# Optimization experiments

Measured on AMD Instinct MI355X. Metric: run time of the kernel, lower is better.

## Reference

```python
import jax, jax.numpy as jnp
import numpy as np

DIM = 1024
HEADS = 16
NUM_EXPERTS = 8
TOP_K = 2
INNER = 4 * DIM
EPS = 1e-5
NEG = -1e9


def setup_inputs() -> dict:
    key = jax.random.key(0)
    ks = jax.random.split(key, 12)
    s = 0.02
    return {
        "x": jax.random.normal(ks[0], (4, 1024, DIM), dtype=jnp.float32),
        "qkv_w": jax.random.normal(ks[1], (DIM, 3 * DIM), dtype=jnp.float32) * s,
        "out_w": jax.random.normal(ks[2], (DIM, DIM), dtype=jnp.float32) * s,
        "out_b": jnp.zeros((DIM,), dtype=jnp.float32),
        "thresh": jnp.float32(-2.0),
        "ln1_g": jnp.ones((DIM,), dtype=jnp.float32),
        "ln1_b": jnp.zeros((DIM,), dtype=jnp.float32),
        "ln2_g": jnp.ones((DIM,), dtype=jnp.float32),
        "ln2_b": jnp.zeros((DIM,), dtype=jnp.float32),
        "gate_w": jax.random.normal(ks[3], (DIM, NUM_EXPERTS), dtype=jnp.float32) * s,
        "w1": jax.random.normal(ks[4], (NUM_EXPERTS, DIM, INNER), dtype=jnp.float32) * s,
        "b1": jnp.zeros((NUM_EXPERTS, INNER), dtype=jnp.float32),
        "w2": jax.random.normal(ks[5], (NUM_EXPERTS, INNER, DIM), dtype=jnp.float32) * s,
        "b2": jnp.zeros((NUM_EXPERTS, DIM), dtype=jnp.float32),
    }


def _layernorm(x, g, b):
    mu = jnp.mean(x, axis=-1, keepdims=True)
    var = jnp.mean(jnp.square(x - mu), axis=-1, keepdims=True)
    return (x - mu) * jax.lax.rsqrt(var + EPS) * g + b


def reference(x, qkv_w, out_w, out_b, thresh, ln1_g, ln1_b, ln2_g, ln2_b,
              gate_w, w1, b1, w2, b2):
    B, N, D = x.shape
    H = HEADS
    Dh = D // H
    scale = Dh ** -0.5

    # --- Sparse attention (pre-norm, eval mode: dropout off) ---
    h = _layernorm(x, ln1_g, ln1_b)
    qkv = h @ qkv_w                                   # [B,N,3D]
    q, k, v = jnp.split(qkv, 3, axis=-1)
    def heads(t):
        return t.reshape(B, N, H, Dh).transpose(0, 2, 1, 3)  # [B,H,N,Dh]
    q, k, v = heads(q), heads(k), heads(v)
    dots = jnp.einsum("bhid,bhjd->bhij", q, k) * scale
    dots = jnp.where(dots < thresh, jnp.float32(NEG), dots)  # learnable sparsity
    attn = jax.nn.softmax(dots, axis=-1)
    o = jnp.einsum("bhij,bhjd->bhid", attn, v)
    o = o.transpose(0, 2, 1, 3).reshape(B, N, D)
    x = x + o @ out_w + out_b

    # --- MoE FFN (pre-norm) ---
    h2 = _layernorm(x, ln2_g, ln2_b).reshape(-1, D)   # [T,D]
    T = h2.shape[0]
    logits = h2 @ gate_w                              # [T,E]
    probs = jax.nn.softmax(logits, axis=-1)
    aux_loss = NUM_EXPERTS * jnp.sum(probs.mean(0) * probs.sum(0))

    top_w, top_i = jax.lax.top_k(logits, TOP_K)       # [T,k]
    top_w = jax.nn.softmax(top_w, axis=-1)
    # dense combine weights: [T,E], zero for unselected experts
    combine = jnp.zeros((T, NUM_EXPERTS), dtype=h2.dtype)
    combine = combine.at[jnp.arange(T)[:, None], top_i].set(top_w)

    out = jnp.zeros_like(h2)
    for e in range(NUM_EXPERTS):
        y = jax.nn.gelu(h2 @ w1[e] + b1[e], approximate=False) @ w2[e] + b2[e]
        out = out + combine[:, e:e + 1] * y

    x = x + out.reshape(B, N, D)
    return x, aux_loss
```

## Files before the change

### kernel.cpp

```cpp
#include <hip/hip_runtime.h>
#include <math.h>

#define DIM 1024
#define THREE_DIM 3072
#define INNER 4096
#define NTOK 4096
#define NPAIR 8192
#define NEXP 8
#define MAXMB 72

typedef __attribute__((ext_vector_type(8))) short bf16x8;
typedef __attribute__((ext_vector_type(4))) float f32x4;

__device__ __forceinline__ unsigned short f2bf(float f){
    unsigned int x = __float_as_uint(f);
    unsigned int r = x + 0x7fffu + ((x >> 16) & 1u);
    return (unsigned short)(r >> 16);
}

__device__ __forceinline__ unsigned short us4c(ushort4 v, int i){
    return i == 0 ? v.x : (i == 1 ? v.y : (i == 2 ? v.z : v.w));
}

__device__ __forceinline__ void glds16(const void* g, void* l){
    __builtin_amdgcn_global_load_lds(
        (const __attribute__((address_space(1))) void*)g,
        (__attribute__((address_space(3))) void*)l, 16, 0, 0);
}

template<int WRITE_BF>
__global__ __launch_bounds__(256)
void ln_kernel(const float* __restrict__ X, const float* __restrict__ g,
               const float* __restrict__ b, float* __restrict__ outF,
               unsigned short* __restrict__ outB)
{
    int row = blockIdx.x;
    int t = threadIdx.x;
    const float4 v = *((const float4*)(X + (size_t)row*DIM) + t);
    float s = v.x + v.y + v.z + v.w;
    #pragma unroll
    for (int m = 1; m < 64; m <<= 1) s += __shfl_xor(s, m, 64);
    __shared__ float red[8];
    int wid = t >> 6, lane = t & 63;
    if (lane == 0) red[wid] = s;
    __syncthreads();
    float mu = (red[0]+red[1]+red[2]+red[3]) * (1.0f/DIM);
    float dx = v.x-mu, dy = v.y-mu, dz = v.z-mu, dw = v.w-mu;
    float s2 = dx*dx + dy*dy + dz*dz + dw*dw;
    #pragma unroll
    for (int m = 1; m < 64; m <<= 1) s2 += __shfl_xor(s2, m, 64);
    if (lane == 0) red[4+wid] = s2;
    __syncthreads();
    float var = (red[4]+red[5]+red[6]+red[7]) * (1.0f/DIM);
    float inv = rsqrtf(var + 1e-5f);
    const float4 gg = *((const float4*)g + t);
    const float4 bb = *((const float4*)b + t);
    float y0 = dx*inv*gg.x + bb.x;
    float y1 = dy*inv*gg.y + bb.y;
    float y2 = dz*inv*gg.z + bb.z;
    float y3 = dw*inv*gg.w + bb.w;
    if (outF){
        float4 o; o.x=y0; o.y=y1; o.z=y2; o.w=y3;
        *((float4*)(outF + (size_t)row*DIM) + t) = o;
    }
    if (WRITE_BF){
        ushort4 u; u.x=f2bf(y0); u.y=f2bf(y1); u.z=f2bf(y2); u.w=f2bf(y3);
        *((ushort4*)(outB + (size_t)row*DIM) + t) = u;
    }
}

template<int MODE>
__global__ __launch_bounds__(256)
void gemm_bf(const unsigned short* __restrict__ A,
             const unsigned short* __restrict__ BT,
             int K, int N,
             const float* __restrict__ bias, const float* __restrict__ resid,
             unsigned short* __restrict__ outB, float* __restrict__ outF)
{
    __shared__ __align__(16) unsigned short As[128*64];
    __shared__ __align__(16) unsigned short Bs[128*64];
    int t = threadIdx.x, lane = t & 63, wid = t >> 6;
    int m0 = blockIdx.y * 128, n0 = blockIdx.x * 128;
    size_t aoff[4], boff[4];
    #pragma unroll
    for (int it = 0; it < 4; ++it){
        int chunk = it*256 + wid*64 + lane;
        int r = chunk >> 3, c16 = chunk & 7;
        int c16s = c16 ^ (r & 7);
        aoff[it] = (size_t)(m0 + r)*K + (size_t)(c16s*8);
        boff[it] = (size_t)(n0 + r)*K + (size_t)(c16s*8);
    }
    int wm = wid >> 1, wn = wid & 1;
    f32x4 acc[4][4];
    #pragma unroll
    for (int mi = 0; mi < 4; ++mi)
        #pragma unroll
        for (int ni = 0; ni < 4; ++ni)
            #pragma unroll
            for (int q = 0; q < 4; ++q) acc[mi][ni][q] = 0.f;

    for (int k0 = 0; k0 < K; k0 += 64){
        __syncthreads();
        #pragma unroll
        for (int it = 0; it < 4; ++it){
            glds16(A  + aoff[it] + k0, As + (size_t)(it*256 + wid*64)*8);
            glds16(BT + boff[it] + k0, Bs + (size_t)(it*256 + wid*64)*8);
        }
        __syncthreads();
        bf16x8 af[4][2], bg[4][2];
        #pragma unroll
        for (int mi = 0; mi < 4; ++mi){
            int row = wm*64 + mi*16 + (lane & 15);
            #pragma unroll
            for (int ks = 0; ks < 2; ++ks){
                int cg = (ks*4 + (lane >> 4)) ^ (row & 7);
                af[mi][ks] = *(const bf16x8*)&As[row*64 + cg*8];
            }
        }
        #pragma unroll
        for (int ni = 0; ni < 4; ++ni){
            int row = wn*64 + ni*16 + (lane & 15);
            #pragma unroll
            for (int ks = 0; ks < 2; ++ks){
                int cg = (ks*4 + (lane >> 4)) ^ (row & 7);
                bg[ni][ks] = *(const bf16x8*)&Bs[row*64 + cg*8];
            }
        }
        #pragma unroll
        for (int ks = 0; ks < 2; ++ks)
            #pragma unroll
            for (int mi = 0; mi < 4; ++mi)
                #pragma unroll
                for (int ni = 0; ni < 4; ++ni)
                    acc[mi][ni] = __builtin_amdgcn_mfma_f32_16x16x32_bf16(
                                      af[mi][ks], bg[ni][ks], acc[mi][ni], 0, 0, 0);
    }
    #pragma unroll
    for (int mi = 0; mi < 4; ++mi){
        #pragma unroll
        for (int ni = 0; ni < 4; ++ni){
            int ccol = n0 + wn*64 + ni*16 + (lane & 15);
            #pragma unroll
            for (int j = 0; j < 4; ++j){
                int row = m0 + wm*64 + mi*16 + (lane >> 4)*4 + j;
                float v = acc[mi][ni][j];
                if (MODE == 0){
                    outB[(size_t)row*N + ccol] = f2bf(v);
                } else {
                    outF[(size_t)row*N + ccol] =
                        v + bias[ccol] + resid[(size_t)row*N + ccol];
                }
            }
        }
    }
}

__global__ __launch_bounds__(256)
void attn4_kernel(const unsigned short* __restrict__ qkv,
                  unsigned short* __restrict__ O,
                  const float* __restrict__ threshp)
{
    __shared__ __align__(16) unsigned short Qs[64*64];
    __shared__ __align__(16) unsigned short Ks[64*64];
    __shared__ __align__(16) unsigned short Vp[8*520];
    __shared__ __align__(16) unsigned short Ps[4*1024];

    int t = threadIdx.x, lane = t & 63, w = t >> 6;
    int arow = lane & 15, agrp = lane >> 4;
    int qt = blockIdx.x, hh = blockIdx.y, bb = blockIdx.z;
    int qrow0 = bb*1024 + qt*64;
    float thresh = threshp[0];

    #pragma unroll
    for (int it = 0; it < 2; ++it){
        int chunk = it*256 + w*64 + lane;
        int r = chunk >> 3, c16 = chunk & 7;
        glds16(qkv + (size_t)(qrow0+r)*3072 + hh*64 + ((c16 ^ (r & 7))*8),
               Qs + (size_t)(it*256 + w*64)*8);
    }
    __syncthreads();
    bf16x8 qf[2];
    {
        int row = w*16 + arow;
        #pragma unroll
        for (int s = 0; s < 2; ++s){
            int c = (s*4 + agrp) ^ (row & 7);
            qf[s] = *(const bf16x8*)&Qs[row*64 + c*8];
        }
    }

    float m_[4], l_[4];
    f32x4 acc[4];
    #pragma unroll
    for (int j = 0; j < 4; ++j){ m_[j] = -INFINITY; l_[j] = 0.f; }
    #pragma unroll
    for (int d4 = 0; d4 < 4; ++d4)
        #pragma unroll
        for (int j = 0; j < 4; ++j) acc[d4][j] = 0.f;

    for (int kt = 0; kt < 16; ++kt){
        __syncthreads();
        int krow0 = bb*1024 + kt*64;
        #pragma unroll
        for (int it = 0; it < 2; ++it){
            int chunk = it*256 + w*64 + lane;
            int r = chunk >> 3, c16 = chunk & 7;
            glds16(qkv + (size_t)(krow0+r)*3072 + 1024 + hh*64 + ((c16 ^ (r & 7))*8),
                   Ks + (size_t)(it*256 + w*64)*8);
        }
        if (t < 128){
            int jc = t & 7, d0 = (t >> 3) * 4;
            ushort4 u[8];
            #pragma unroll
            for (int jj = 0; jj < 8; ++jj)
                u[jj] = *(const ushort4*)(qkv + (size_t)(krow0 + jc*8 + jj)*3072
                                          + 2048 + hh*64 + d0);
            #pragma unroll
            for (int i = 0; i < 4; ++i){
                ushort4 a, b;
                a.x = us4c(u[0], i); a.y = us4c(u[1], i);
                a.z = us4c(u[2], i); a.w = us4c(u[3], i);
                b.x = us4c(u[4], i); b.y = us4c(u[5], i);
                b.z = us4c(u[6], i); b.w = us4c(u[7], i);
                *(ushort4*)&Vp[jc*520 + (d0+i)*8]     = a;
                *(ushort4*)&Vp[jc*520 + (d0+i)*8 + 4] = b;
            }
        }
        __syncthreads();

        f32x4 sv[4];
        #pragma unroll
        for (int n = 0; n < 4; ++n)
            #pragma unroll
            for (int j = 0; j < 4; ++j) sv[n][j] = 0.f;
        #pragma unroll
        for (int n = 0; n < 4; ++n){
            int krow = n*16 + arow;
            #pragma unroll
            for (int s = 0; s < 2; ++s){
                int c = (s*4 + agrp) ^ (krow & 7);
                bf16x8 kf = *(const bf16x8*)&Ks[krow*64 + c*8];
                sv[n] = __builtin_amdgcn_mfma_f32_16x16x32_bf16(qf[s], kf, sv[n], 0, 0, 0);
            }
        }
        #pragma unroll
        for (int n = 0; n < 4; ++n)
            #pragma unroll
            for (int j = 0; j < 4; ++j){
                float s = sv[n][j] * 0.125f;
                sv[n][j] = (s < thresh) ? -1e9f : s;
            }
        float tmax[4], fac[4], rsum[4];
        #pragma unroll
        for (int j = 0; j < 4; ++j)
            tmax[j] = fmaxf(fmaxf(sv[0][j], sv[1][j]), fmaxf(sv[2][j], sv[3][j]));
        #pragma unroll
        for (int msk = 1; msk < 16; msk <<= 1)
            #pragma unroll
            for (int j = 0; j < 4; ++j)
                tmax[j] = fmaxf(tmax[j], __shfl_xor(tmax[j], msk, 64));
        #pragma unroll
        for (int j = 0; j < 4; ++j){
            float mn = fmaxf(m_[j], tmax[j]);
            fac[j] = __expf(m_[j] - mn);
            m_[j] = mn;
        }
        #pragma unroll
        for (int n = 0; n < 4; ++n)
            #pragma unroll
            for (int j = 0; j < 4; ++j)
                sv[n][j] = __expf(sv[n][j] - m_[j]);
        #pragma unroll
        for (int j = 0; j < 4; ++j)
            rsum[j] = sv[0][j] + sv[1][j] + sv[2][j] + sv[3][j];
        #pragma unroll
        for (int msk = 1; msk < 16; msk <<= 1)
            #pragma unroll
            for (int j = 0; j < 4; ++j)
                rsum[j] += __shfl_xor(rsum[j], msk, 64);
        #pragma unroll
        for (int j = 0; j < 4; ++j)
            l_[j] = l_[j]*fac[j] + rsum[j];
        #pragma unroll
        for (int n = 0; n < 4; ++n){
            int col = n*16 + arow;
            #pragma unroll
            for (int j = 0; j < 4; ++j){
                int r = agrp*4 + j;
                int idx = r*64 + (((col>>3) ^ (r&7)) << 3) + (col & 7);
                Ps[w*1024 + idx] = f2bf(sv[n][j]);
            }
        }
        #pragma unroll
        for (int d4 = 0; d4 < 4; ++d4)
            #pragma unroll
            for (int j = 0; j < 4; ++j) acc[d4][j] *= fac[j];
        #pragma unroll
        for (int s = 0; s < 2; ++s){
            int c = (s*4 + agrp) ^ (arow & 7);
            bf16x8 pa = *(const bf16x8*)&Ps[w*1024 + arow*64 + c*8];
            int jc = s*4 + agrp;
            #pragma unroll
            for (int d4 = 0; d4 < 4; ++d4){
                int dcol = d4*16 + arow;
                bf16x8 vb = *(const bf16x8*)&Vp[jc*520 + dcol*8];
                acc[d4] = __builtin_amdgcn_mfma_f32_16x16x32_bf16(pa, vb, acc[d4], 0, 0, 0);
            }
        }
    }
    #pragma unroll
    for (int j = 0; j < 4; ++j){
        float inv = 1.0f / l_[j];
        int row = qrow0 + w*16 + agrp*4 + j;
        #pragma unroll
        for (int d4 = 0; d4 < 4; ++d4)
            O[(size_t)row*1024 + hh*64 + d4*16 + arow] = f2bf(acc[d4][j] * inv);
    }
}

__global__ __launch_bounds__(64)
void gate_kernel(const float* __restrict__ h2, const float* __restrict__ gw,
                 float* __restrict__ probs, int* __restrict__ top_i,
                 float* __restrict__ top_w)
{
    int tk = blockIdx.x;
    int lane = threadIdx.x;
    const float* hr = h2 + (size_t)tk*DIM;
    float acc[8];
    #pragma unroll
    for (int e = 0; e < 8; ++e) acc[e] = 0.f;
    for (int d = lane; d < DIM; d += 64){
        float hv = hr[d];
        const float* grow = gw + d*8;
        #pragma unroll
        for (int e = 0; e < 8; ++e) acc[e] = fmaf(hv, grow[e], acc[e]);
    }
    #pragma unroll
    for (int m = 1; m < 64; m <<= 1)
        #pragma unroll
        for (int e = 0; e < 8; ++e) acc[e] += __shfl_xor(acc[e], m, 64);
    if (lane == 0){
        float mx = acc[0];
        #pragma unroll
        for (int e = 1; e < 8; ++e) mx = fmaxf(mx, acc[e]);
        float p[8], s = 0.f;
        #pragma unroll
        for (int e = 0; e < 8; ++e){ p[e] = __expf(acc[e]-mx); s += p[e]; }
        float invs = 1.f/s;
        #pragma unroll
        for (int e = 0; e < 8; ++e) probs[(size_t)tk*8+e] = p[e]*invs;
        int i0 = 0; float v0 = acc[0];
        #pragma unroll
        for (int e = 1; e < 8; ++e) if (acc[e] > v0){ v0 = acc[e]; i0 = e; }
        int i1 = -1; float v1 = -INFINITY;
        #pragma unroll
        for (int e = 0; e < 8; ++e) if (e != i0 && acc[e] > v1){ v1 = acc[e]; i1 = e; }
        float w0 = 1.f/(1.f + __expf(v1 - v0));
        top_i[tk*2]   = i0; top_i[tk*2+1] = i1;
        top_w[tk*2]   = w0; top_w[tk*2+1] = 1.f - w0;
    }
}

__global__ __launch_bounds__(256)
void aux_kernel(const float* __restrict__ probs, float* __restrict__ dout)
{
    int t = threadIdx.x;
    float acc[8];
    #pragma unroll
    for (int e = 0; e < 8; ++e) acc[e] = 0.f;
    for (int r = t; r < NTOK; r += 256){
        const float* pr = probs + (size_t)r*8;
        #pragma unroll
        for (int e = 0; e < 8; ++e) acc[e] += pr[e];
    }
    #pragma unroll
    for (int m = 1; m < 64; m <<= 1)
        #pragma unroll
        for (int e = 0; e < 8; ++e) acc[e] += __shfl_xor(acc[e], m, 64);
    __shared__ float red[4][8];
    int wid = t >> 6, lane = t & 63;
    if (lane == 0)
        for (int e = 0; e < 8; ++e) red[wid][e] = acc[e];
    __syncthreads();
    if (t == 0){
        float aux = 0.f;
        for (int e = 0; e < 8; ++e){
            float S = red[0][e]+red[1][e]+red[2][e]+red[3][e];
            aux += S*S;
        }
        dout[(size_t)NTOK*DIM] = aux * (8.0f/NTOK);
    }
}

__global__ __launch_bounds__(512)
void routing_kernel(const int* __restrict__ topi, int* __restrict__ perm,
                    int* __restrict__ mblk_e)
{
    __shared__ int cnt[8];
    __shared__ int obase[8];
    int t = threadIdx.x, w = t >> 6, lane = t & 63;
    int c = 0;
    for (int i0 = 0; i0 < NPAIR; i0 += 64){
        int e = topi[i0 + lane];
        c += (e == w) ? 1 : 0;
    }
    #pragma unroll
    for (int m = 1; m < 64; m <<= 1) c += __shfl_xor(c, m, 64);
    if (lane == 0) cnt[w] = c;
    __syncthreads();
    if (t == 0){
        int mb = 0;
        for (int e = 0; e < 8; ++e){
            obase[e] = mb*128;
            int nb = (cnt[e] + 127) >> 7;
            for (int k = 0; k < nb; ++k) mblk_e[mb++] = e;
        }
        for (; mb < MAXMB; ++mb) mblk_e[mb] = -1;
    }
    __syncthreads();
    for (int i = t; i < MAXMB*128; i += 512) perm[i] = -1;
    __syncthreads();
    int base = obase[w];
    for (int i0 = 0; i0 < NPAIR; i0 += 64){
        int p = i0 + lane;
        int e = topi[p];
        bool mt = (e == w);
        unsigned long long mk = __ballot(mt);
        int rank = __popcll(mk & ((1ull << lane) - 1ull));
        if (mt) perm[base + rank] = p;
        base += __popcll(mk);
    }
}

template<int MODE>
__global__ __launch_bounds__(256)
void gemm_moe2(const unsigned short* __restrict__ Abase,
               const unsigned short* __restrict__ BTbase,
               int K, int N, int lda,
               const int* __restrict__ perm, const int* __restrict__ mblk_e,
               const float* __restrict__ bias,
               unsigned short* __restrict__ actout,
               const float* __restrict__ topw, float* __restrict__ dout)
{
    int mb = blockIdx.y;
    int e = mblk_e[mb];
    if (e < 0) return;
    __shared__ __align__(16) unsigned short As[128*64];
    __shared__ __align__(16) unsigned short Bs[128*64];
    __shared__ int permL[128];
    int t = threadIdx.x;
    if (t < 128) permL[t] = perm[mb*128 + t];
    __syncthreads();
    int lane = t & 63, wid = t >> 6;
    int n0 = blockIdx.x * 128;
    const unsigned short* BT = BTbase + (size_t)e * (size_t)N * (size_t)K;
    int base_chunk = wid*64 + lane;
    size_t aoff[4], boff[4];
    #pragma unroll
    for (int it = 0; it < 4; ++it){
        int chunk = base_chunk + it*256;
        int r = chunk >> 3, c16 = chunk & 7;
        int c16s = c16 ^ (r & 7);
        size_t ar;
        if (MODE == 2){ int p = permL[r]; ar = (p >= 0) ? (size_t)(p >> 1) : 0; }
        else          { ar = (size_t)(mb*128 + r); }
        aoff[it] = ar*(size_t)lda + (size_t)(c16s*8);
        boff[it] = (size_t)(n0 + r)*(size_t)K + (size_t)(c16s*8);
    }
    int wm = wid >> 1, wn = wid & 1;
    f32x4 acc[4][4];
    #pragma unroll
    for (int mi = 0; mi < 4; ++mi)
        #pragma unroll
        for (int ni = 0; ni < 4; ++ni)
            #pragma unroll
            for (int q = 0; q < 4; ++q) acc[mi][ni][q] = 0.f;

    for (int k0 = 0; k0 < K; k0 += 64){
        __syncthreads();
        #pragma unroll
        for (int it = 0; it < 4; ++it){
            glds16(Abase + aoff[it] + k0, As + (size_t)(wid*64 + it*256)*8);
            glds16(BT    + boff[it] + k0, Bs + (size_t)(wid*64 + it*256)*8);
        }
        __syncthreads();
        bf16x8 af[4][2], bg[4][2];
        #pragma unroll
        for (int mi = 0; mi < 4; ++mi){
            int row = wm*64 + mi*16 + (lane & 15);
            #pragma unroll
            for (int ks = 0; ks < 2; ++ks){
                int cg = (ks*4 + (lane >> 4)) ^ (row & 7);
                af[mi][ks] = *(const bf16x8*)&As[row*64 + cg*8];
            }
        }
        #pragma unroll
        for (int ni = 0; ni < 4; ++ni){
            int row = wn*64 + ni*16 + (lane & 15);
            #pragma unroll
            for (int ks = 0; ks < 2; ++ks){
                int cg = (ks*4 + (lane >> 4)) ^ (row & 7);
                bg[ni][ks] = *(const bf16x8*)&Bs[row*64 + cg*8];
            }
        }
        #pragma unroll
        for (int ks = 0; ks < 2; ++ks)
            #pragma unroll
            for (int mi = 0; mi < 4; ++mi)
                #pragma unroll
                for (int ni = 0; ni < 4; ++ni)
                    acc[mi][ni] = __builtin_amdgcn_mfma_f32_16x16x32_bf16(
                                      af[mi][ks], bg[ni][ks], acc[mi][ni], 0, 0, 0);
    }
    #pragma unroll
    for (int mi = 0; mi < 4; ++mi){
        #pragma unroll
        for (int ni = 0; ni < 4; ++ni){
            int ccol = n0 + wn*64 + ni*16 + (lane & 15);
            float bv = bias[(size_t)e*N + ccol];
            #pragma unroll
            for (int j = 0; j < 4; ++j){
                int rloc = wm*64 + mi*16 + (lane >> 4)*4 + j;
                float v = acc[mi][ni][j];
                if (MODE == 2){
                    float gx = v + bv;
                    float z2 = gx * fmaf(gx*gx, 0.07135481283f, 1.595769122f);
                    float ex = __expf(-z2);
                    float gl = gx * __builtin_amdgcn_rcpf(1.0f + ex);
                    actout[(size_t)(mb*128 + rloc)*N + ccol] = f2bf(gl);
                } else {
                    int p = permL[rloc];
                    if (p >= 0){
                        float val = (v + bv) * topw[p];
                        atomicAdd(&dout[(size_t)(p >> 1)*N + ccol], val);
                    }
                }
            }
        }
    }
}

__global__ __launch_bounds__(256)
void transp_cast(const float* __restrict__ W, unsigned short* __restrict__ WT,
                 int K, int N)
{
    __shared__ float tile[32][33];
    size_t base = (size_t)blockIdx.z * (size_t)K * (size_t)N;
    const float* Wp = W + base;
    unsigned short* Tp = WT + base;
    int t = threadIdx.x;
    int r = t >> 3, c4 = (t & 7) << 2;
    int n0 = blockIdx.x << 5, k0 = blockIdx.y << 5;
    float4 v = *(const float4*)(Wp + (size_t)(k0+r)*N + n0 + c4);
    tile[r][c4+0] = v.x; tile[r][c4+1] = v.y;
    tile[r][c4+2] = v.z; tile[r][c4+3] = v.w;
    __syncthreads();
    ushort4 u;
    u.x = f2bf(tile[c4+0][r]);
    u.y = f2bf(tile[c4+1][r]);
    u.z = f2bf(tile[c4+2][r]);
    u.w = f2bf(tile[c4+3][r]);
    *(ushort4*)(Tp + (size_t)(n0+r)*K + k0 + c4) = u;
}

extern "C" void kernel_launch(void* const* d_in, const int* in_sizes, int n_in,
                              void* d_out, int out_size, void* d_ws, size_t ws_size,
                              hipStream_t stream)
{
    const float* x      = (const float*)d_in[0];
    const float* qkv_w  = (const float*)d_in[1];
    const float* out_w  = (const float*)d_in[2];
    const float* out_b  = (const float*)d_in[3];
    const float* thresh = (const float*)d_in[4];
    const float* ln1_g  = (const float*)d_in[5];
    const float* ln1_b  = (const float*)d_in[6];
    const float* ln2_g  = (const float*)d_in[7];
    const float* ln2_b  = (const float*)d_in[8];
    const float* gate_w = (const float*)d_in[9];
    const float* w1     = (const float*)d_in[10];
    const float* b1     = (const float*)d_in[11];
    const float* w2     = (const float*)d_in[12];
    const float* b2     = (const float*)d_in[13];
    float* out = (float*)d_out;
    char* ws = (char*)d_ws;

    const size_t MB = (size_t)1 << 20;
    unsigned short* h1bf  = (unsigned short*)(ws);
    unsigned short* qkvbf = (unsigned short*)(ws + 8*MB);
    unsigned short* obf   = (unsigned short*)(ws + 32*MB);
    float*          h2    = (float*)(ws + 40*MB);
    unsigned short* h2bf  = (unsigned short*)(ws + 56*MB);
    unsigned short* qwT   = (unsigned short*)(ws + 64*MB);
    unsigned short* owT   = (unsigned short*)(ws + 70*MB);
    unsigned short* w1T   = (unsigned short*)(ws + 72*MB);
    unsigned short* w2T   = (unsigned short*)(ws + 136*MB);
    unsigned short* act   = (unsigned short*)(ws + 200*MB);
    float* probs          = (float*)(ws + 276*MB);
    int*   top_i          = (int*)(ws + 276*MB + 131072);
    float* top_w          = (float*)(ws + 276*MB + 163840);
    int*   perm           = (int*)(ws + 276*MB + 196608);
    int*   mblk           = (int*)(ws + 276*MB + 237568);

    transp_cast<<<dim3(THREE_DIM/32, DIM/32, 1), 256, 0, stream>>>(qkv_w, qwT, DIM, THREE_DIM);
    transp_cast<<<dim3(DIM/32, DIM/32, 1), 256, 0, stream>>>(out_w, owT, DIM, DIM);

    ln_kernel<1><<<NTOK, 256, 0, stream>>>(x, ln1_g, ln1_b, nullptr, h1bf);
    gemm_bf<0><<<dim3(THREE_DIM/128, NTOK/128), 256, 0, stream>>>(
        h1bf, qwT, DIM, THREE_DIM, nullptr, nullptr, qkvbf, nullptr);
    attn4_kernel<<<dim3(16, 16, 4), 256, 0, stream>>>(qkvbf, obf, thresh);
    gemm_bf<1><<<dim3(DIM/128, NTOK/128), 256, 0, stream>>>(
        obf, owT, DIM, DIM, out_b, x, nullptr, out);
    ln_kernel<1><<<NTOK, 256, 0, stream>>>(out, ln2_g, ln2_b, h2, h2bf);
    gate_kernel<<<NTOK, 64, 0, stream>>>(h2, gate_w, probs, top_i, top_w);
    aux_kernel<<<1, 256, 0, stream>>>(probs, out);
    routing_kernel<<<1, 512, 0, stream>>>(top_i, perm, mblk);

    transp_cast<<<dim3(INNER/32, DIM/32, NEXP), 256, 0, stream>>>(w1, w1T, DIM, INNER);
    transp_cast<<<dim3(DIM/32, INNER/32, NEXP), 256, 0, stream>>>(w2, w2T, INNER, DIM);

    gemm_moe2<2><<<dim3(INNER/128, MAXMB), 256, 0, stream>>>(
        h2bf, w1T, DIM, INNER, DIM, perm, mblk, b1, act, nullptr, nullptr);
    gemm_moe2<3><<<dim3(DIM/128, MAXMB), 256, 0, stream>>>(
        act, w2T, INNER, DIM, INNER, perm, mblk, b2, nullptr, top_w, out);
}
```

Measured before the change: 513.3 us.

## Swizzle block IDs across XCDs and split-K the MoE down-projection

Flattens the launch grids of the GEMMs and the attention kernel to 1D and remaps block IDs so that consecutive logical tiles land on the same XCD, aiming for better L2 reuse of shared A/B tiles across the MI355X's chiplets. The second MoE GEMM is also split along K into two halves, doubling its grid to improve occupancy. The split is safe because that GEMM already accumulates with atomics, and bias is added only by the first split. The cost is extra atomic traffic on the output and some index arithmetic per block.

Measured after the change: 553.1 us. 7.7% more time.

```diff
diff --git a/kernel.cpp b/kernel.cpp
--- a/kernel.cpp
+++ b/kernel.cpp
@@ -26,6 +26,11 @@
     __builtin_amdgcn_global_load_lds(
         (const __attribute__((address_space(1))) void*)g,
         (__attribute__((address_space(3))) void*)l, 16, 0, 0);
+}
+
+__device__ __forceinline__ int xcd_swz(){
+    int cpx = gridDim.x >> 3;
+    return (blockIdx.x & 7) * cpx + (blockIdx.x >> 3);
 }
 
 template<int WRITE_BF>
@@ -73,14 +78,16 @@
 __global__ __launch_bounds__(256)
 void gemm_bf(const unsigned short* __restrict__ A,
              const unsigned short* __restrict__ BT,
-             int K, int N,
+             int K, int N, int gnx,
              const float* __restrict__ bias, const float* __restrict__ resid,
              unsigned short* __restrict__ outB, float* __restrict__ outF)
 {
     __shared__ __align__(16) unsigned short As[128*64];
     __shared__ __align__(16) unsigned short Bs[128*64];
+    int fid = xcd_swz();
+    int nx = fid % gnx, my = fid / gnx;
+    int m0 = my * 128, n0 = nx * 128;
     int t = threadIdx.x, lane = t & 63, wid = t >> 6;
-    int m0 = blockIdx.y * 128, n0 = blockIdx.x * 128;
     size_t aoff[4], boff[4];
     #pragma unroll
     for (int it = 0; it < 4; ++it){
@@ -165,9 +172,10 @@
     __shared__ __align__(16) unsigned short Vp[8*520];
     __shared__ __align__(16) unsigned short Ps[4*1024];
 
+    int fid = xcd_swz();
+    int qt = fid & 15, hh = (fid >> 4) & 15, bb = fid >> 8;
     int t = threadIdx.x, lane = t & 63, w = t >> 6;
     int arow = lane & 15, agrp = lane >> 4;
-    int qt = blockIdx.x, hh = blockIdx.y, bb = blockIdx.z;
     int qrow0 = bb*1024 + qt*64;
     float thresh = threshp[0];
 
@@ -442,9 +450,17 @@
                unsigned short* __restrict__ actout,
                const float* __restrict__ topw, float* __restrict__ dout)
 {
-    int mb = blockIdx.y;
+    const int GNX = (MODE == 2) ? (INNER/128) : (DIM/128);
+    const int KSP = (MODE == 2) ? 1 : 2;
+    int fid = xcd_swz();
+    int nx = fid % GNX;
+    int rest = fid / GNX;
+    int mb = rest % MAXMB;
+    int kk = rest / MAXMB;
     int e = mblk_e[mb];
     if (e < 0) return;
+    int kspan = K / KSP, kbeg = kk * kspan, kend = kbeg + kspan;
+
     __shared__ __align__(16) unsigned short As[128*64];
     __shared__ __align__(16) unsigned short Bs[128*64];
     __shared__ int permL[128];
@@ -452,7 +468,7 @@
     if (t < 128) permL[t] = perm[mb*128 + t];
     __syncthreads();
     int lane = t & 63, wid = t >> 6;
-    int n0 = blockIdx.x * 128;
+    int n0 = nx * 128;
     const unsigned short* BT = BTbase + (size_t)e * (size_t)N * (size_t)K;
     int base_chunk = wid*64 + lane;
     size_t aoff[4], boff[4];
@@ -476,7 +492,7 @@
             #pragma unroll
             for (int q = 0; q < 4; ++q) acc[mi][ni][q] = 0.f;
 
-    for (int k0 = 0; k0 < K; k0 += 64){
+    for (int k0 = kbeg; k0 < kend; k0 += 64){
         __syncthreads();
         #pragma unroll
         for (int it = 0; it < 4; ++it){
@@ -517,7 +533,7 @@
         #pragma unroll
         for (int ni = 0; ni < 4; ++ni){
             int ccol = n0 + wn*64 + ni*16 + (lane & 15);
-            float bv = bias[(size_t)e*N + ccol];
+            float bv = (kk == 0) ? bias[(size_t)e*N + ccol] : 0.f;
             #pragma unroll
             for (int j = 0; j < 4; ++j){
                 int rloc = wm*64 + mi*16 + (lane >> 4)*4 + j;
@@ -605,11 +621,11 @@
     transp_cast<<<dim3(DIM/32, DIM/32, 1), 256, 0, stream>>>(out_w, owT, DIM, DIM);
 
     ln_kernel<1><<<NTOK, 256, 0, stream>>>(x, ln1_g, ln1_b, nullptr, h1bf);
-    gemm_bf<0><<<dim3(THREE_DIM/128, NTOK/128), 256, 0, stream>>>(
-        h1bf, qwT, DIM, THREE_DIM, nullptr, nullptr, qkvbf, nullptr);
-    attn4_kernel<<<dim3(16, 16, 4), 256, 0, stream>>>(qkvbf, obf, thresh);
-    gemm_bf<1><<<dim3(DIM/128, NTOK/128), 256, 0, stream>>>(
-        obf, owT, DIM, DIM, out_b, x, nullptr, out);
+    gemm_bf<0><<<(THREE_DIM/128)*(NTOK/128), 256, 0, stream>>>(
+        h1bf, qwT, DIM, THREE_DIM, THREE_DIM/128, nullptr, nullptr, qkvbf, nullptr);
+    attn4_kernel<<<16*16*4, 256, 0, stream>>>(qkvbf, obf, thresh);
+    gemm_bf<1><<<(DIM/128)*(NTOK/128), 256, 0, stream>>>(
+        obf, owT, DIM, DIM, DIM/128, out_b, x, nullptr, out);
     ln_kernel<1><<<NTOK, 256, 0, stream>>>(out, ln2_g, ln2_b, h2, h2bf);
     gate_kernel<<<NTOK, 64, 0, stream>>>(h2, gate_w, probs, top_i, top_w);
     aux_kernel<<<1, 256, 0, stream>>>(probs, out);
@@ -618,8 +634,8 @@
     transp_cast<<<dim3(INNER/32, DIM/32, NEXP), 256, 0, stream>>>(w1, w1T, DIM, INNER);
     transp_cast<<<dim3(DIM/32, INNER/32, NEXP), 256, 0, stream>>>(w2, w2T, INNER, DIM);
 
-    gemm_moe2<2><<<dim3(INNER/128, MAXMB), 256, 0, stream>>>(
+    gemm_moe2<2><<<(INNER/128)*MAXMB, 256, 0, stream>>>(
         h2bf, w1T, DIM, INNER, DIM, perm, mblk, b1, act, nullptr, nullptr);
-    gemm_moe2<3><<<dim3(DIM/128, MAXMB), 256, 0, stream>>>(
+    gemm_moe2<3><<<(DIM/128)*MAXMB*2, 256, 0, stream>>>(
         act, w2T, INNER, DIM, INNER, perm, mblk, b2, nullptr, top_w, out);
 }
```
